# Kernel optimization log

Measured on AMD Instinct MI355X. Metric: run time of the kernel, lower is better.

The kernel has to match this reference:

```python
import jax, jax.numpy as jnp
import numpy as np

B, F = 512, 512
K, D = 32, 16  # num_kernels, dim_per_kernel


def setup_inputs() -> dict:
    key = jax.random.key(0)
    kx, kt = jax.random.split(key)
    x = jax.random.normal(kx, (B, F), dtype=jnp.float32)
    # keras 'uniform' init is small-range uniform; scale similarly
    T = jax.random.uniform(kt, (F, K * D), dtype=jnp.float32, minval=-0.05, maxval=0.05)
    return {"x": x, "T": T}


def reference(x, T):
    # m: [B, K, D]
    m = (x @ T).reshape(-1, K, D)
    # all-pairs L1 distance per kernel: [B, B, K]
    abs_diffs = jnp.sum(jnp.abs(m[:, None, :, :] - m[None, :, :, :]), axis=-1)
    # minibatch features: sum_j exp(-||m_i - m_j||_1) -> [B, K]
    feats = jnp.sum(jnp.exp(-abs_diffs), axis=1)
    return jnp.concatenate([x, feats], axis=1)
```

## Files before the change

### kernel.cpp

```cpp
#include <hip/hip_runtime.h>
#include <math.h>

#define BSZ 512
#define FDIM 512
#define NK 32
#define DD 16
#define NDIM (NK*DD)
#define OUTW (FDIM + NK)

__global__ __launch_bounds__(512) void k_gemm(
    const float* __restrict__ x, const float* __restrict__ T,
    float* __restrict__ m, float* __restrict__ out) {
  const int t  = threadIdx.x;
  const int b  = blockIdx.x;
  const int rg = b >> 3;
  const int cg = b & 7;
  const int lane = t & 63;
  const int w    = __builtin_amdgcn_readfirstlane(t >> 6);
  const int col  = cg * 64 + lane;
  const int r0   = rg * 8;
  const int k0   = w * 64;

  float acc[8];
#pragma unroll
  for (int r = 0; r < 8; ++r) acc[r] = 0.f;

  const float* __restrict__ Tp = T + (size_t)k0 * NDIM + col;
  const float* __restrict__ xp = x + (size_t)r0 * FDIM + k0;
#pragma unroll 8
  for (int k = 0; k < 64; ++k) {
    const float tv = Tp[(size_t)k * NDIM];
#pragma unroll
    for (int r = 0; r < 8; ++r)
      acc[r] = fmaf(xp[(size_t)r * FDIM + k], tv, acc[r]);
  }

  __shared__ float red[8][8][64];
#pragma unroll
  for (int r = 0; r < 8; ++r) red[w][r][lane] = acc[r];
  __syncthreads();
  {
    const int rr = t >> 6;
    float s = 0.f;
#pragma unroll
    for (int ww = 0; ww < 8; ++ww) s += red[ww][rr][lane];
    m[(size_t)(r0 + rr) * NDIM + col] = s;
  }

  const int g = b * 512 + t;
  if (g < 65536) {
    const int orow = g >> 7, c4 = g & 127;
    *(float4*)(out + (size_t)orow * OUTW + c4 * 4) =
        *(const float4*)(x + (size_t)orow * FDIM + c4 * 4);
  } else if (g < 65536 + 16384) {
    const int idx = g - 65536;
    const int orow = idx >> 5, kk = idx & 31;
    out[(size_t)orow * OUTW + FDIM + kk] = 0.f;
  }
}

__global__ __launch_bounds__(256) void k_dist(
    const float* __restrict__ m, float* __restrict__ out) {
  __shared__ float Bs[128 * DD];
  __shared__ float red[256];
  const int t   = threadIdx.x;
  const int bid = blockIdx.x;
  const int ig  = bid >> 7;
  const int k   = (bid >> 2) & 31;
  const int jq  = bid & 3;
  const int lane = t & 63;
  const int i    = ig * 64 + lane;

  const float4* ap = (const float4*)(m + (size_t)i * NDIM + k * DD);
  const float4 A0 = ap[0], A1 = ap[1], A2 = ap[2], A3 = ap[3];

  const float* mb = m + (size_t)(jq * 128) * NDIM + k * DD;
#pragma unroll
  for (int q = 0; q < 2; ++q) {
    const int idx = q * 256 + t;
    const int jrow = idx >> 2, part = idx & 3;
    *(float4*)&Bs[jrow * DD + part * 4] =
        *(const float4*)(mb + (size_t)jrow * NDIM + part * 4);
  }
  __syncthreads();

  float a[DD];
  a[0]=A0.x; a[1]=A0.y; a[2]=A0.z;  a[3]=A0.w;
  a[4]=A1.x; a[5]=A1.y; a[6]=A1.z;  a[7]=A1.w;
  a[8]=A2.x; a[9]=A2.y; a[10]=A2.z; a[11]=A2.w;
  a[12]=A3.x;a[13]=A3.y;a[14]=A3.z; a[15]=A3.w;

  const int w = __builtin_amdgcn_readfirstlane(t >> 6);
  const int jbase = w * 32;
  float f = 0.f;
#pragma unroll 4
  for (int j = 0; j < 32; ++j) {
    const float4* bp = (const float4*)&Bs[(jbase + j) * DD];
    const float4 b0 = bp[0], b1 = bp[1], b2 = bp[2], b3 = bp[3];
    float d =
        fabsf(a[0]  - b0.x) + fabsf(a[1]  - b0.y) +
        fabsf(a[2]  - b0.z) + fabsf(a[3]  - b0.w) +
        fabsf(a[4]  - b1.x) + fabsf(a[5]  - b1.y) +
        fabsf(a[6]  - b1.z) + fabsf(a[7]  - b1.w) +
        fabsf(a[8]  - b2.x) + fabsf(a[9]  - b2.y) +
        fabsf(a[10] - b2.z) + fabsf(a[11] - b2.w) +
        fabsf(a[12] - b3.x) + fabsf(a[13] - b3.y) +
        fabsf(a[14] - b3.z) + fabsf(a[15] - b3.w);
    f += __expf(-d);
  }

  red[t] = f;
  __syncthreads();
  if (t < 64) {
    const float s = red[t] + red[t + 64] + red[t + 128] + red[t + 192];
    atomicAdd(out + (size_t)(ig * 64 + t) * OUTW + FDIM + k, s);
  }
}

extern "C" void kernel_launch(void* const* d_in, const int* in_sizes, int n_in,
                              void* d_out, int out_size, void* d_ws,
                              size_t ws_size, hipStream_t stream) {
  (void)in_sizes; (void)n_in; (void)out_size; (void)ws_size;
  const float* x = (const float*)d_in[0];
  const float* T = (const float*)d_in[1];
  float* out = (float*)d_out;
  float* m   = (float*)d_ws;

  hipLaunchKernelGGL(k_gemm, dim3(512), dim3(512), 0, stream, x, T, m, out);
  hipLaunchKernelGGL(k_dist, dim3(1024), dim3(256), 0, stream, m, out);
}
```

Baseline: 74.00 us.

## Compute projection GEMM with bf16 MFMA instead of fp32 FMA loops

Replaces the scalar fp32 GEMM with bf16 16x16x32 MFMA instructions: each wave covers a quarter of the K dimension for a 16x16 output tile, and the partial sums are reduced through shared memory. The launch changes to 1024 blocks of 256 threads. The aim is to cut GEMM time through matrix cores. Inputs are rounded to bf16, which perturbs m and the exp-of-distance features and risks accuracy.

New measurement: 72.36 us. -2.2%, faster.

```diff
diff --git a/kernel.cpp b/kernel.cpp
--- a/kernel.cpp
+++ b/kernel.cpp
@@ -1,4 +1,5 @@
 #include <hip/hip_runtime.h>
+#include <hip/hip_bf16.h>
 #include <math.h>
 
 #define BSZ 512
@@ -8,46 +9,56 @@
 #define NDIM (NK*DD)
 #define OUTW (FDIM + NK)
 
-__global__ __launch_bounds__(512) void k_gemm(
+typedef __attribute__((ext_vector_type(8))) short short8;
+typedef __attribute__((ext_vector_type(4))) float float4v;
+
+static __device__ __forceinline__ short f2bf(float f) {
+  return (short)__builtin_bit_cast(unsigned short, __float2bfloat16(f));
+}
+
+__global__ __launch_bounds__(256) void k_gemm(
     const float* __restrict__ x, const float* __restrict__ T,
     float* __restrict__ m, float* __restrict__ out) {
   const int t  = threadIdx.x;
   const int b  = blockIdx.x;
-  const int rg = b >> 3;
-  const int cg = b & 7;
+  const int rg = b >> 5, cg = b & 31;
+  const int r0 = rg * 16, c0 = cg * 16;
   const int lane = t & 63;
   const int w    = __builtin_amdgcn_readfirstlane(t >> 6);
-  const int col  = cg * 64 + lane;
-  const int r0   = rg * 8;
-  const int k0   = w * 64;
+  const int mi   = lane & 15;
+  const int q    = lane >> 4;
 
-  float acc[8];
+  const float* __restrict__ xa = x + (size_t)(r0 + mi) * FDIM + 128 * w + 8 * q;
+  const float* __restrict__ tb = T + (size_t)(128 * w + 8 * q) * NDIM + c0 + mi;
+
+  float4v acc = {0.f, 0.f, 0.f, 0.f};
 #pragma unroll
-  for (int r = 0; r < 8; ++r) acc[r] = 0.f;
-
-  const float* __restrict__ Tp = T + (size_t)k0 * NDIM + col;
-  const float* __restrict__ xp = x + (size_t)r0 * FDIM + k0;
-#pragma unroll 8
-  for (int k = 0; k < 64; ++k) {
-    const float tv = Tp[(size_t)k * NDIM];
+  for (int j = 0; j < 4; ++j) {
+    const float4 a0 = *(const float4*)(xa + 32 * j);
+    const float4 a1 = *(const float4*)(xa + 32 * j + 4);
+    float bv[8];
 #pragma unroll
-    for (int r = 0; r < 8; ++r)
-      acc[r] = fmaf(xp[(size_t)r * FDIM + k], tv, acc[r]);
+    for (int i = 0; i < 8; ++i) bv[i] = tb[(size_t)(32 * j + i) * NDIM];
+    short8 af, bf;
+    af[0] = f2bf(a0.x); af[1] = f2bf(a0.y); af[2] = f2bf(a0.z); af[3] = f2bf(a0.w);
+    af[4] = f2bf(a1.x); af[5] = f2bf(a1.y); af[6] = f2bf(a1.z); af[7] = f2bf(a1.w);
+#pragma unroll
+    for (int i = 0; i < 8; ++i) bf[i] = f2bf(bv[i]);
+    acc = __builtin_amdgcn_mfma_f32_16x16x32_bf16(af, bf, acc, 0, 0, 0);
   }
 
-  __shared__ float red[8][8][64];
+  __shared__ float red[4][16][16];
 #pragma unroll
-  for (int r = 0; r < 8; ++r) red[w][r][lane] = acc[r];
+  for (int r = 0; r < 4; ++r) red[w][q * 4 + r][mi] = acc[r];
   __syncthreads();
   {
-    const int rr = t >> 6;
-    float s = 0.f;
-#pragma unroll
-    for (int ww = 0; ww < 8; ++ww) s += red[ww][rr][lane];
-    m[(size_t)(r0 + rr) * NDIM + col] = s;
+    const int orow = t >> 4, ocol = t & 15;
+    const float s = red[0][orow][ocol] + red[1][orow][ocol] +
+                    red[2][orow][ocol] + red[3][orow][ocol];
+    m[(size_t)(r0 + orow) * NDIM + c0 + ocol] = s;
   }
 
-  const int g = b * 512 + t;
+  const int g = b * 256 + t;
   if (g < 65536) {
     const int orow = g >> 7, c4 = g & 127;
     *(float4*)(out + (size_t)orow * OUTW + c4 * 4) =
@@ -76,8 +87,8 @@
 
   const float* mb = m + (size_t)(jq * 128) * NDIM + k * DD;
 #pragma unroll
-  for (int q = 0; q < 2; ++q) {
-    const int idx = q * 256 + t;
+  for (int qq = 0; qq < 2; ++qq) {
+    const int idx = qq * 256 + t;
     const int jrow = idx >> 2, part = idx & 3;
     *(float4*)&Bs[jrow * DD + part * 4] =
         *(const float4*)(mb + (size_t)jrow * NDIM + part * 4);
@@ -126,6 +137,6 @@
   float* out = (float*)d_out;
   float* m   = (float*)d_ws;
 
-  hipLaunchKernelGGL(k_gemm, dim3(512), dim3(512), 0, stream, x, T, m, out);
+  hipLaunchKernelGGL(k_gemm, dim3(1024), dim3(256), 0, stream, x, T, m, out);
   hipLaunchKernelGGL(k_dist, dim3(1024), dim3(256), 0, stream, m, out);
 }
```
